# Kernel optimization log

Measured on AMD Instinct MI355X. Metric: run time of the kernel, lower is better.

The kernel has to match this reference:

```python
import jax, jax.numpy as jnp
import numpy as np

NTIME = 20      # number of time blocks
V = 128         # vehicle_num per time block
F_OUT = 128     # out_features (== in_features here)
ALPHA = 0.2     # LeakyReLU negative slope
NEG = -9e15     # mask fill value used by the torch module


def setup_inputs() -> dict:
    key = jax.random.key(0)
    k1, k2, k3, k4 = jax.random.split(key, 4)
    h = jax.random.normal(k1, (NTIME * V, F_OUT), dtype=jnp.float32)
    # binary adjacency mask, broadcast over the feature dim like the torch code
    adj = jax.random.randint(k2, (V, V, 1), 0, 2).astype(jnp.float32)
    share_weight = jax.random.normal(k3, (F_OUT, F_OUT), dtype=jnp.float32) * 0.05
    a = jax.random.normal(k4, (2 * F_OUT, F_OUT), dtype=jnp.float32) * 0.05
    return {"h": h, "adj": adj, "share_weight": share_weight, "a": a}


def reference(h, adj, share_weight, a):
    # Wh: [N, F]
    Wh = h @ share_weight
    # a_input @ a decomposes: e[p,q,:] = leakyrelu(Wh[p] @ a[:F] + Wh[q] @ a[F:])
    # Only the block-diagonal (per-time) slices of e are ever used, so compute
    # blocks directly instead of the full NxNxF tensor.
    a1, a2 = a[:F_OUT], a[F_OUT:]
    e1 = (Wh @ a1).reshape(NTIME, V, F_OUT)  # [T, v, F]
    e2 = (Wh @ a2).reshape(NTIME, V, F_OUT)
    e = e1[:, :, None, :] + e2[:, None, :, :]           # [T, v, v, F]
    e = jnp.where(e > 0, e, ALPHA * e)                   # LeakyReLU
    masked = jnp.where(adj[None] > 0, e, NEG)            # mask per time block
    # torch softmax(dim=1) on [v, v, F] blocks -> axis=2 here (the j index)
    attention_raw = jax.nn.softmax(masked, axis=2)       # [T, v, v, F]
    # training=False => dropout is identity.
    # h_prime[t,b,f] = sum_j att[t,b,j,f] * Wh[t,j,f]  (the diagonal-of-matmul trick)
    Whb = Wh.reshape(NTIME, V, F_OUT)
    h_prime = jnp.einsum('tbjf,tjf->tbf', attention_raw, Whb)
    out = jax.nn.elu(h_prime)                            # concat=True branch
    return (out, attention_raw)
```

## Files before the change

### kernel.cpp

```cpp
#include <hip/hip_runtime.h>
#include <hip/hip_bf16.h>
#include <math.h>

#define NTIME 20
#define V 128
#define F 128
constexpr float ALPHA = 0.2f;

__global__ __launch_bounds__(128) void k_wa(const float* __restrict__ W,
                                            const float* __restrict__ a,
                                            float* __restrict__ Wa) {
  const int i = blockIdx.x;
  const int s = blockIdx.y;
  const int k = threadIdx.x;
  __shared__ float wrow[F];
  wrow[k] = W[i * F + k];
  __syncthreads();
  const float* as = a + s * F * F;
  float acc = 0.f;
#pragma unroll 8
  for (int m = 0; m < F; ++m) acc += wrow[m] * as[m * F + k];
  Wa[(s * F + i) * F + k] = acc;
}

__global__ __launch_bounds__(256) void k_gemm(const float* __restrict__ h,
                                              const float* __restrict__ W,
                                              const float* __restrict__ Wa,
                                              float* __restrict__ Wh,
                                              float* __restrict__ E1,
                                              float* __restrict__ E2) {
  __shared__ float Alds[64][129];
  __shared__ float Blds[128][64];
  const int tid = threadIdx.x;
  const int rb = blockIdx.x * 64;
  const int matc = blockIdx.y >> 1;
  const int cb = (blockIdx.y & 1) * 64;

#pragma unroll
  for (int p = 0; p < 8; ++p) {
    int id = tid + p * 256;
    int row = id >> 5;
    int c0 = (id & 31) * 4;
    float4 v = *reinterpret_cast<const float4*>(&h[(rb + row) * F + c0]);
    Alds[row][c0 + 0] = v.x; Alds[row][c0 + 1] = v.y;
    Alds[row][c0 + 2] = v.z; Alds[row][c0 + 3] = v.w;
  }
  const float* src = (matc == 0) ? W : (Wa + (matc - 1) * F * F);
#pragma unroll
  for (int p = 0; p < 8; ++p) {
    int id = tid + p * 256;
    int k = id >> 4;
    int c0 = (id & 15) * 4;
    float4 v = *reinterpret_cast<const float4*>(&src[k * F + cb + c0]);
    Blds[k][c0 + 0] = v.x; Blds[k][c0 + 1] = v.y;
    Blds[k][c0 + 2] = v.z; Blds[k][c0 + 3] = v.w;
  }
  __syncthreads();

  const int tx = tid & 15;
  const int ty = tid >> 4;
  float acc[4][4] = {};
#pragma unroll 4
  for (int k = 0; k < 128; ++k) {
    float4 bv = *reinterpret_cast<const float4*>(&Blds[k][tx * 4]);
    float a0 = Alds[ty * 4 + 0][k];
    float a1 = Alds[ty * 4 + 1][k];
    float a2 = Alds[ty * 4 + 2][k];
    float a3 = Alds[ty * 4 + 3][k];
    acc[0][0] += a0 * bv.x; acc[0][1] += a0 * bv.y; acc[0][2] += a0 * bv.z; acc[0][3] += a0 * bv.w;
    acc[1][0] += a1 * bv.x; acc[1][1] += a1 * bv.y; acc[1][2] += a1 * bv.z; acc[1][3] += a1 * bv.w;
    acc[2][0] += a2 * bv.x; acc[2][1] += a2 * bv.y; acc[2][2] += a2 * bv.z; acc[2][3] += a2 * bv.w;
    acc[3][0] += a3 * bv.x; acc[3][1] += a3 * bv.y; acc[3][2] += a3 * bv.z; acc[3][3] += a3 * bv.w;
  }

  float* Dp = (matc == 0) ? Wh : ((matc == 1) ? E1 : E2);
  const int gr0 = rb + ty * 4;
  const int c0 = cb + tx * 4;
#pragma unroll
  for (int i = 0; i < 4; ++i) {
    float4 v;
    v.x = acc[i][0]; v.y = acc[i][1]; v.z = acc[i][2]; v.w = acc[i][3];
    *reinterpret_cast<float4*>(&Dp[(gr0 + i) * F + c0]) = v;
  }
}

__global__ __launch_bounds__(256) void k_attn(const float* __restrict__ Wh,
                                              const float* __restrict__ E1,
                                              const float* __restrict__ E2,
                                              const float* __restrict__ adj,
                                              float* __restrict__ out,
                                              float* __restrict__ att) {
  const int wid = threadIdx.x >> 6;
  const int lane = threadIdx.x & 63;
  const int r = blockIdx.x * 4 + wid;
  const int t = r >> 7;
  const int b = r & 127;
  const int fc = lane * 2;

  const float2 e1v = *reinterpret_cast<const float2*>(E1 + r * F + fc);
  const float* E2t = E2 + t * V * F;
  const float* Wht = Wh + t * V * F;
  const float* adjb = adj + b * V;

  float s0 = 0.f, s1 = 0.f, h0 = 0.f, h1 = 0.f;
#pragma unroll 4
  for (int j = 0; j < V; ++j) {
    if (adjb[j] > 0.f) {
      float2 e2 = *reinterpret_cast<const float2*>(E2t + j * F + fc);
      float x0 = e1v.x + e2.x, x1 = e1v.y + e2.y;
      x0 = x0 > 0.f ? x0 : ALPHA * x0;
      x1 = x1 > 0.f ? x1 : ALPHA * x1;
      float p0 = __expf(x0), p1 = __expf(x1);
      float2 w = *reinterpret_cast<const float2*>(Wht + j * F + fc);
      s0 += p0; s1 += p1;
      h0 += p0 * w.x; h1 += p1 * w.y;
    }
  }
  const bool uni = (s0 == 0.f);
  if (uni) {
    s0 = s1 = (float)V;
    for (int j = 0; j < V; ++j) {
      float2 w = *reinterpret_cast<const float2*>(Wht + j * F + fc);
      h0 += w.x; h1 += w.y;
    }
  }
  const float inv0 = 1.f / s0, inv1 = 1.f / s1;

  float* attb = att + (size_t)r * (V * F);
#pragma unroll 4
  for (int j = 0; j < V; ++j) {
    float2 o;
    if (uni) {
      o.x = inv0; o.y = inv1;
    } else if (adjb[j] > 0.f) {
      float2 e2 = *reinterpret_cast<const float2*>(E2t + j * F + fc);
      float x0 = e1v.x + e2.x, x1 = e1v.y + e2.y;
      x0 = x0 > 0.f ? x0 : ALPHA * x0;
      x1 = x1 > 0.f ? x1 : ALPHA * x1;
      o.x = __expf(x0) * inv0;
      o.y = __expf(x1) * inv1;
    } else {
      o.x = 0.f; o.y = 0.f;
    }
    *reinterpret_cast<float2*>(attb + j * F + fc) = o;
  }

  const float hp0 = h0 * inv0, hp1 = h1 * inv1;
  float2 ov;
  ov.x = hp0 > 0.f ? hp0 : __expf(hp0) - 1.f;
  ov.y = hp1 > 0.f ? hp1 : __expf(hp1) - 1.f;
  *reinterpret_cast<float2*>(out + r * F + fc) = ov;
}

extern "C" void kernel_launch(void* const* d_in, const int* in_sizes, int n_in,
                              void* d_out, int out_size, void* d_ws, size_t ws_size,
                              hipStream_t stream) {
  (void)in_sizes; (void)n_in; (void)out_size; (void)ws_size;
  const float* h   = (const float*)d_in[0];
  const float* adj = (const float*)d_in[1];
  const float* W   = (const float*)d_in[2];
  const float* a   = (const float*)d_in[3];

  float* Wh = (float*)d_ws;
  float* E1 = Wh + NTIME * V * F;
  float* E2 = E1 + NTIME * V * F;
  float* Wa = E2 + NTIME * V * F;

  float* out = (float*)d_out;
  float* att = out + NTIME * V * F;

  k_wa<<<dim3(128, 2), 128, 0, stream>>>(W, a, Wa);
  k_gemm<<<dim3(40, 6), 256, 0, stream>>>(h, W, Wa, Wh, E1, E2);
  k_attn<<<dim3(640), 256, 0, stream>>>(Wh, E1, E2, adj, out, att);
}
```

Baseline: 246.1 us.

## Split attention row across four waves over j with shared-memory reduction

Each block now handles a single output row instead of four, and its four waves each cover a quarter of the neighbour index j. Partial softmax sums are combined through shared memory. The attention write pass switches to float4 stores and computes the exp without a branch, masking the result afterwards. This gives more parallelism and wider stores for the large attention output write, at the cost of extra syncs, a redundant exp on masked entries, and a serial fallback loop run by one wave.

```diff
diff --git a/kernel.cpp b/kernel.cpp
--- a/kernel.cpp
+++ b/kernel.cpp
@@ -90,66 +90,98 @@
                                               const float* __restrict__ adj,
                                               float* __restrict__ out,
                                               float* __restrict__ att) {
-  const int wid = threadIdx.x >> 6;
-  const int lane = threadIdx.x & 63;
-  const int r = blockIdx.x * 4 + wid;
+  __shared__ float sA[4][F];
+  __shared__ float hA[4][F];
+  __shared__ float invA[F];
+
+  const int r = blockIdx.x;
   const int t = r >> 7;
   const int b = r & 127;
+  const int w = threadIdx.x >> 6;
+  const int lane = threadIdx.x & 63;
   const int fc = lane * 2;
-
-  const float2 e1v = *reinterpret_cast<const float2*>(E1 + r * F + fc);
+  const int j0 = w * 32;
+
   const float* E2t = E2 + t * V * F;
   const float* Wht = Wh + t * V * F;
   const float* adjb = adj + b * V;
+  const float2 e1v = *reinterpret_cast<const float2*>(E1 + r * F + fc);
 
   float s0 = 0.f, s1 = 0.f, h0 = 0.f, h1 = 0.f;
 #pragma unroll 4
-  for (int j = 0; j < V; ++j) {
+  for (int jj = 0; jj < 32; ++jj) {
+    const int j = j0 + jj;
     if (adjb[j] > 0.f) {
       float2 e2 = *reinterpret_cast<const float2*>(E2t + j * F + fc);
       float x0 = e1v.x + e2.x, x1 = e1v.y + e2.y;
       x0 = x0 > 0.f ? x0 : ALPHA * x0;
       x1 = x1 > 0.f ? x1 : ALPHA * x1;
       float p0 = __expf(x0), p1 = __expf(x1);
-      float2 w = *reinterpret_cast<const float2*>(Wht + j * F + fc);
+      float2 wv = *reinterpret_cast<const float2*>(Wht + j * F + fc);
       s0 += p0; s1 += p1;
-      h0 += p0 * w.x; h1 += p1 * w.y;
+      h0 += p0 * wv.x; h1 += p1 * wv.y;
     }
   }
-  const bool uni = (s0 == 0.f);
-  if (uni) {
-    s0 = s1 = (float)V;
-    for (int j = 0; j < V; ++j) {
-      float2 w = *reinterpret_cast<const float2*>(Wht + j * F + fc);
-      h0 += w.x; h1 += w.y;
+  sA[w][fc] = s0; sA[w][fc + 1] = s1;
+  hA[w][fc] = h0; hA[w][fc + 1] = h1;
+  __syncthreads();
+
+  const float S0 = sA[0][fc] + sA[1][fc] + sA[2][fc] + sA[3][fc];
+  const float S1 = sA[0][fc + 1] + sA[1][fc + 1] + sA[2][fc + 1] + sA[3][fc + 1];
+  const bool uni = (S0 == 0.f);
+  const float inv0 = uni ? (1.f / (float)V) : (1.f / S0);
+  const float inv1 = uni ? (1.f / (float)V) : (1.f / S1);
+  if (w == 0) { invA[fc] = inv0; invA[fc + 1] = inv1; }
+
+  if (w == 0) {
+    float H0, H1;
+    if (uni) {
+      H0 = 0.f; H1 = 0.f;
+      for (int j = 0; j < V; ++j) {
+        float2 wv = *reinterpret_cast<const float2*>(Wht + j * F + fc);
+        H0 += wv.x; H1 += wv.y;
+      }
+      H0 *= inv0; H1 *= inv1;
+    } else {
+      H0 = (hA[0][fc] + hA[1][fc] + hA[2][fc] + hA[3][fc]) * inv0;
+      H1 = (hA[0][fc + 1] + hA[1][fc + 1] + hA[2][fc + 1] + hA[3][fc + 1]) * inv1;
     }
-  }
-  const float inv0 = 1.f / s0, inv1 = 1.f / s1;
-
+    float2 ov;
+    ov.x = H0 > 0.f ? H0 : __expf(H0) - 1.f;
+    ov.y = H1 > 0.f ? H1 : __expf(H1) - 1.f;
+    *reinterpret_cast<float2*>(out + r * F + fc) = ov;
+  }
+  __syncthreads();
+
+  const int jh = lane >> 5;
+  const int f4 = (lane & 31) * 4;
+  const float4 e1q = *reinterpret_cast<const float4*>(E1 + r * F + f4);
+  const float4 invq = *reinterpret_cast<const float4*>(&invA[f4]);
   float* attb = att + (size_t)r * (V * F);
+
 #pragma unroll 4
-  for (int j = 0; j < V; ++j) {
-    float2 o;
+  for (int jj = 0; jj < 16; ++jj) {
+    const int j = j0 + jj * 2 + jh;
+    const float av = adjb[j];
+    const float4 e2q = *reinterpret_cast<const float4*>(E2t + j * F + f4);
+    float x0 = e1q.x + e2q.x, x1 = e1q.y + e2q.y;
+    float x2 = e1q.z + e2q.z, x3 = e1q.w + e2q.w;
+    x0 = x0 > 0.f ? x0 : ALPHA * x0;
+    x1 = x1 > 0.f ? x1 : ALPHA * x1;
+    x2 = x2 > 0.f ? x2 : ALPHA * x2;
+    x3 = x3 > 0.f ? x3 : ALPHA * x3;
+    float4 o;
+    o.x = __expf(x0) * invq.x;
+    o.y = __expf(x1) * invq.y;
+    o.z = __expf(x2) * invq.z;
+    o.w = __expf(x3) * invq.w;
     if (uni) {
-      o.x = inv0; o.y = inv1;
-    } else if (adjb[j] > 0.f) {
-      float2 e2 = *reinterpret_cast<const float2*>(E2t + j * F + fc);
-      float x0 = e1v.x + e2.x, x1 = e1v.y + e2.y;
-      x0 = x0 > 0.f ? x0 : ALPHA * x0;
-      x1 = x1 > 0.f ? x1 : ALPHA * x1;
-      o.x = __expf(x0) * inv0;
-      o.y = __expf(x1) * inv1;
-    } else {
-      o.x = 0.f; o.y = 0.f;
+      o.x = invq.x; o.y = invq.y; o.z = invq.z; o.w = invq.w;
+    } else if (av <= 0.f) {
+      o.x = 0.f; o.y = 0.f; o.z = 0.f; o.w = 0.f;
     }
-    *reinterpret_cast<float2*>(attb + j * F + fc) = o;
-  }
-
-  const float hp0 = h0 * inv0, hp1 = h1 * inv1;
-  float2 ov;
-  ov.x = hp0 > 0.f ? hp0 : __expf(hp0) - 1.f;
-  ov.y = hp1 > 0.f ? hp1 : __expf(hp1) - 1.f;
-  *reinterpret_cast<float2*>(out + r * F + fc) = ov;
+    *reinterpret_cast<float4*>(attb + j * F + f4) = o;
+  }
 }
 
 extern "C" void kernel_launch(void* const* d_in, const int* in_sizes, int n_in,
@@ -171,5 +203,5 @@
 
   k_wa<<<dim3(128, 2), 128, 0, stream>>>(W, a, Wa);
   k_gemm<<<dim3(40, 6), 256, 0, stream>>>(h, W, Wa, Wh, E1, E2);
-  k_attn<<<dim3(640), 256, 0, stream>>>(Wh, E1, E2, adj, out, att);
-}
+  k_attn<<<dim3(NTIME * V), 256, 0, stream>>>(Wh, E1, E2, adj, out, att);
+}
```

Measured after the change: 210.3 us. -14.5%, faster.
